# Kernel tuning notes

Hardware: AMD Instinct MI355X
Metric: run time of the kernel (lower is better)

The kernel has to match this reference:

```python
import jax, jax.numpy as jnp
import numpy as np

D_MODEL = 1024
N_HEADS = 16
D_K = D_MODEL // N_HEADS
D_FF = 4096
EPS = 1e-6
NEG = -1e9


def layer_norm(x, alpha, bias):
    # torch: mean/std over last dim, std is unbiased (ddof=1), eps added to std
    mean = jnp.mean(x, axis=-1, keepdims=True)
    std = jnp.std(x, axis=-1, keepdims=True, ddof=1)
    return alpha * (x - mean) / (std + EPS) + bias


def setup_inputs() -> dict:
    key = jax.random.key(0)
    ks = jax.random.split(key, 12)
    B, S = 2, 2048
    s_attn = 1.0 / np.sqrt(D_MODEL)
    s_ff1 = 1.0 / np.sqrt(D_MODEL)
    s_ff2 = 1.0 / np.sqrt(D_FF)
    inp = {
        "x": jax.random.normal(ks[0], (B, S, D_MODEL), jnp.float32),
        "mask": jnp.ones((1, 1, S, S), jnp.int32),
        "wq": jax.random.normal(ks[1], (D_MODEL, D_MODEL), jnp.float32) * s_attn,
        "bq": jnp.zeros((D_MODEL,), jnp.float32),
        "wk": jax.random.normal(ks[2], (D_MODEL, D_MODEL), jnp.float32) * s_attn,
        "bk": jnp.zeros((D_MODEL,), jnp.float32),
        "wv": jax.random.normal(ks[3], (D_MODEL, D_MODEL), jnp.float32) * s_attn,
        "bv": jnp.zeros((D_MODEL,), jnp.float32),
        "wo": jax.random.normal(ks[4], (D_MODEL, D_MODEL), jnp.float32) * s_attn,
        "bo": jnp.zeros((D_MODEL,), jnp.float32),
        "w1": jax.random.normal(ks[5], (D_MODEL, D_FF), jnp.float32) * s_ff1,
        "b1": jnp.zeros((D_FF,), jnp.float32),
        "w2": jax.random.normal(ks[6], (D_FF, D_MODEL), jnp.float32) * s_ff2,
        "b2": jnp.zeros((D_MODEL,), jnp.float32),
        "a1": jnp.ones((1,), jnp.float32),
        "c1": jnp.zeros((1,), jnp.float32),
        "a2": jnp.ones((1,), jnp.float32),
        "c2": jnp.zeros((1,), jnp.float32),
    }
    return inp


def reference(x, mask, wq, bq, wk, bk, wv, bv, wo, bo, w1, b1, w2, b2, a1, c1, a2, c2):
    B, S, D = x.shape

    def mha(h):
        q = (h @ wq + bq).reshape(B, S, N_HEADS, D_K).transpose(0, 2, 1, 3)
        k = (h @ wk + bk).reshape(B, S, N_HEADS, D_K).transpose(0, 2, 1, 3)
        v = (h @ wv + bv).reshape(B, S, N_HEADS, D_K).transpose(0, 2, 1, 3)
        scores = jnp.einsum('bhqd,bhkd->bhqk', q, k) / jnp.sqrt(jnp.float32(D_K))
        scores = jnp.where(mask == 0, jnp.float32(NEG), scores)
        weights = jax.nn.softmax(scores, axis=-1)
        out = jnp.einsum('bhqk,bhkd->bhqd', weights, v)
        out = out.transpose(0, 2, 1, 3).reshape(B, S, D)
        return out @ wo + bo

    def ffn(h):
        return jax.nn.relu(h @ w1 + b1) @ w2 + b2

    # pre-LN residual connections (dropout=0 / eval mode)
    x = x + mha(layer_norm(x, a1, c1))
    x = x + ffn(layer_norm(x, a2, c2))
    return x
```

## Files before the change

kernel.cpp:

```cpp
#include <hip/hip_runtime.h>
#include <hip/hip_bf16.h>
#include <type_traits>


typedef __attribute__((ext_vector_type(8))) short short8v;
typedef __attribute__((ext_vector_type(4))) float f32x4;
typedef __attribute__((ext_vector_type(4))) unsigned uint4v;

#define D_MODEL 1024
#define SEQ 2048
#define NROWS 4096

__device__ __forceinline__ short f2bs(float f) {
  __hip_bfloat16 h = __float2bfloat16(f);
  return __builtin_bit_cast(short, h);
}

__device__ __forceinline__ unsigned cvtpk(float lo, float hi) {
  unsigned r;
  asm("v_cvt_pk_bf16_f32 %0, %1, %2" : "=v"(r) : "v"(lo), "v"(hi));
  return r;
}

__device__ __forceinline__ void perm16swap(unsigned& a, unsigned& b) {
  asm volatile("v_permlane16_swap_b32 %0, %1" : "+v"(a), "+v"(b));
}

__device__ __forceinline__ void async_copy16(const void* g, void* l) {
  __builtin_amdgcn_global_load_lds(
      (__attribute__((address_space(1))) void*)g,
      (__attribute__((address_space(3))) void*)l,
      16, 0, 0);
}

__global__ __launch_bounds__(256)
void transpose4_bf16_kernel(const float* __restrict__ wq, const float* __restrict__ wk,
                            const float* __restrict__ wv, const float* __restrict__ wo,
                            short* __restrict__ oq, short* __restrict__ ow,
                            float qscale) {
  __shared__ float tile[32][33];
  const int z = blockIdx.z;
  const float* in = (z == 0) ? wq : (z == 1) ? wk : (z == 2) ? wv : wo;
  short* out = (z < 3) ? (oq + (size_t)z * 1024 * 1024) : ow;
  const float scale = (z == 0) ? qscale : 1.0f;
  const int n0 = blockIdx.x * 32, k0 = blockIdx.y * 32;
  const int tx = threadIdx.x, ty = threadIdx.y;
#pragma unroll
  for (int j = 0; j < 4; ++j)
    tile[ty + j * 8][tx] = in[(size_t)(k0 + ty + j * 8) * 1024 + n0 + tx];
  __syncthreads();
#pragma unroll
  for (int j = 0; j < 4; ++j)
    out[(size_t)(n0 + ty + j * 8) * 1024 + k0 + tx] = f2bs(tile[tx][ty + j * 8] * scale);
}

__global__ __launch_bounds__(256)
void transpose_ffn_kernel(const float* __restrict__ w1, const float* __restrict__ w2,
                          short* __restrict__ o1, short* __restrict__ o2) {
  __shared__ float tile[32][33];
  const int z = blockIdx.z;
  const float* in = z ? w2 : w1;
  short* out = z ? o2 : o1;
  const int K = z ? 4096 : 1024, N = z ? 1024 : 4096;
  const int n0 = (z ? blockIdx.y : blockIdx.x) * 32;
  const int k0 = (z ? blockIdx.x : blockIdx.y) * 32;
  const int tx = threadIdx.x, ty = threadIdx.y;
#pragma unroll
  for (int j = 0; j < 4; ++j)
    tile[ty + j * 8][tx] = in[(size_t)(k0 + ty + j * 8) * N + n0 + tx];
  __syncthreads();
#pragma unroll
  for (int j = 0; j < 4; ++j)
    out[(size_t)(n0 + ty + j * 8) * K + k0 + tx] = f2bs(tile[tx][ty + j * 8]);
}

__global__ __launch_bounds__(256)
void transpose_v_kernel(const short* __restrict__ qkv, short* __restrict__ vt) {
  __shared__ short tile[32][33];
  const int bh = blockIdx.z, b = bh >> 4, h = bh & 15;
  const int s0 = blockIdx.x * 32, d0 = blockIdx.y * 32;
  const int tx = threadIdx.x, ty = threadIdx.y;
  const short* src = qkv + ((size_t)b * SEQ) * 3072 + 2048 + h * 64;
#pragma unroll
  for (int j = 0; j < 4; ++j)
    tile[ty + j * 8][tx] = src[(size_t)(s0 + ty + j * 8) * 3072 + d0 + tx];
  __syncthreads();
  short* dst = vt + (size_t)bh * 64 * SEQ;
#pragma unroll
  for (int j = 0; j < 4; ++j)
    dst[(size_t)(d0 + ty + j * 8) * SEQ + s0 + tx] = tile[tx][ty + j * 8];
}

__global__ void concat_bias_kernel(const float* __restrict__ bq, const float* __restrict__ bk,
                                   const float* __restrict__ bv, float* __restrict__ outb,
                                   float qscale) {
  int i = blockIdx.x * 256 + threadIdx.x;
  float v = (i < 1024) ? bq[i] * qscale : (i < 2048 ? bk[i - 1024] : bv[i - 2048]);
  outb[i] = v;
}

__global__ __launch_bounds__(256)
void layernorm_kernel(const float* __restrict__ x, short* __restrict__ out,
                      const float* __restrict__ alpha, const float* __restrict__ beta) {
  const int row = blockIdx.x;
  const int t = threadIdx.x;
  float4 v = ((const float4*)(x + (size_t)row * D_MODEL))[t];
  float s = v.x + v.y + v.z + v.w;
  float sq = v.x * v.x + v.y * v.y + v.z * v.z + v.w * v.w;
#pragma unroll
  for (int m = 1; m < 64; m <<= 1) {
    s += __shfl_xor(s, m, 64);
    sq += __shfl_xor(sq, m, 64);
  }
  __shared__ float sh_s[4], sh_q[4];
  const int wid = t >> 6;
  if ((t & 63) == 0) { sh_s[wid] = s; sh_q[wid] = sq; }
  __syncthreads();
  s = sh_s[0] + sh_s[1] + sh_s[2] + sh_s[3];
  sq = sh_q[0] + sh_q[1] + sh_q[2] + sh_q[3];
  const float mean = s * (1.0f / 1024.0f);
  const float var = fmaxf(0.0f, (sq - 1024.0f * mean * mean) * (1.0f / 1023.0f));
  const float scl = alpha[0] / (sqrtf(var) + 1e-6f);
  const float sft = beta[0];
  short4 o;
  o.x = f2bs((v.x - mean) * scl + sft);
  o.y = f2bs((v.y - mean) * scl + sft);
  o.z = f2bs((v.z - mean) * scl + sft);
  o.w = f2bs((v.w - mean) * scl + sft);
  ((short4*)(out + (size_t)row * D_MODEL))[t] = o;
}

template <int MF, int NF, bool RELU, bool RESID, bool OUT_BF16>
__global__ __launch_bounds__(256)
void gemm_bt_sb_kernel(const short* __restrict__ A, const short* __restrict__ Bt,
                       const float* __restrict__ bias, const float* __restrict__ resid,
                       void* __restrict__ out, int M, int N, int K) {
  constexpr int BM = MF * 32, BN = NF * 32, BK = 64;
  __shared__ short As[BM * BK];
  __shared__ short Bs[BN * BK];
  const int tid = threadIdx.x;
  const int lane = tid & 63, wid = tid >> 6;
  const int wr = wid >> 1, wc = wid & 1;
  const int l15 = lane & 15, kg = lane >> 4;

  const int gx = gridDim.x;
  const int nwg = gx * gridDim.y;
  const int bid = blockIdx.y * gx + blockIdx.x;
  const int tilei = (bid & 7) * (nwg >> 3) + (bid >> 3);
  const int m0 = (tilei / gx) * BM, n0 = (tilei % gx) * BN;

  f32x4 acc[MF][NF];
#pragma unroll
  for (int m = 0; m < MF; ++m)
#pragma unroll
    for (int n = 0; n < NF; ++n) acc[m][n] = (f32x4){0.f, 0.f, 0.f, 0.f};

  const int r0 = tid >> 3, c0 = tid & 7;
  const int csw = (c0 ^ (r0 & 7)) << 3;
  const short* pa = A + (size_t)(m0 + r0) * K + csw;
  const short* pb = Bt + (size_t)(n0 + r0) * K + csw;

  const int NT = K / BK;
  for (int t = 0; t < NT; ++t) {
    const size_t ko = (size_t)t * BK;
#pragma unroll
    for (int it = 0; it < MF; ++it)
      async_copy16(pa + (size_t)it * 32 * K + ko, &As[(tid + it * 256) * 8]);
#pragma unroll
    for (int it = 0; it < NF; ++it)
      async_copy16(pb + (size_t)it * 32 * K + ko, &Bs[(tid + it * 256) * 8]);
    __syncthreads();

    short8v a[2][MF], b[2][NF];
#pragma unroll
    for (int m = 0; m < MF; ++m) {
      const int row = wr * MF * 16 + m * 16 + l15;
#pragma unroll
      for (int kt = 0; kt < 2; ++kt)
        a[kt][m] = *(const short8v*)&As[row * BK + (((kg + 4 * kt) ^ (row & 7)) << 3)];
    }
#pragma unroll
    for (int n = 0; n < NF; ++n) {
      const int row = wc * NF * 16 + n * 16 + l15;
#pragma unroll
      for (int kt = 0; kt < 2; ++kt)
        b[kt][n] = *(const short8v*)&Bs[row * BK + (((kg + 4 * kt) ^ (row & 7)) << 3)];
    }
    __builtin_amdgcn_s_setprio(1);
#pragma unroll
    for (int kt = 0; kt < 2; ++kt)
#pragma unroll
      for (int m = 0; m < MF; ++m)
#pragma unroll
        for (int n = 0; n < NF; ++n)
          acc[m][n] = __builtin_amdgcn_mfma_f32_16x16x32_bf16(a[kt][m], b[kt][n], acc[m][n], 0, 0, 0);
    __builtin_amdgcn_s_setprio(0);
    __syncthreads();
  }

#pragma unroll
  for (int m = 0; m < MF; ++m) {
#pragma unroll
    for (int n = 0; n < NF; ++n) {
      const int col = n0 + wc * NF * 16 + n * 16 + l15;
      const float bv = bias[col];
#pragma unroll
      for (int r = 0; r < 4; ++r) {
        const size_t row = (size_t)(m0 + wr * MF * 16 + m * 16 + kg * 4 + r);
        float v = acc[m][n][r] + bv;
        if (RELU) v = fmaxf(v, 0.0f);
        if (RESID) v += resid[row * N + col];
        if (OUT_BF16)
          ((short*)out)[row * N + col] = f2bs(v);
        else
          ((float*)out)[row * N + col] = v;
      }
    }
  }
}

template <bool RELU, bool RESID, bool OUT_BF16>
__global__ __launch_bounds__(256)
void gemm_bt_k64_kernel(const short* __restrict__ A, const short* __restrict__ Bt,
                        const float* __restrict__ bias, const float* __restrict__ resid,
                        void* __restrict__ out, int M, int N, int K) {
  constexpr int BM = 64, BN = 64, BK = 64;
  __shared__ short As[2][BM * BK];
  __shared__ short Bs[2][BN * BK];
  const int tid = threadIdx.x;
  const int lane = tid & 63, wid = tid >> 6;
  const int wr = wid >> 1, wc = wid & 1;
  const int l15 = lane & 15, kg = lane >> 4;

  const int gx = gridDim.x;
  const int nwg = gx * gridDim.y;
  const int bid = blockIdx.y * gx + blockIdx.x;
  const int tilei = (bid & 7) * (nwg >> 3) + (bid >> 3);
  const int m0 = (tilei / gx) * BM, n0 = (tilei % gx) * BN;

  f32x4 acc[2][2];
#pragma unroll
  for (int m = 0; m < 2; ++m)
#pragma unroll
    for (int n = 0; n < 2; ++n) acc[m][n] = (f32x4){0.f, 0.f, 0.f, 0.f};

  const int rA0 = tid >> 3, cA0 = (((tid & 7)) ^ (rA0 & 7)) << 3;
  const int rA1 = (tid + 256) >> 3, cA1 = (((tid + 256) & 7) ^ (rA1 & 7)) << 3;
  const short* pa0 = A + (size_t)(m0 + rA0) * K + cA0;
  const short* pa1 = A + (size_t)(m0 + rA1) * K + cA1;
  const short* pb0 = Bt + (size_t)(n0 + rA0) * K + cA0;
  const short* pb1 = Bt + (size_t)(n0 + rA1) * K + cA1;

  auto stage = [&](int buf, int t) {
    const size_t ko = (size_t)t * BK;
    async_copy16(pa0 + ko, &As[buf][tid * 8]);
    async_copy16(pa1 + ko, &As[buf][(tid + 256) * 8]);
    async_copy16(pb0 + ko, &Bs[buf][tid * 8]);
    async_copy16(pb1 + ko, &Bs[buf][(tid + 256) * 8]);
  };

  const int NT = K / BK;

  auto bodyk = [&](auto BUFC, int t) {
    constexpr int buf = decltype(BUFC)::value;
    if (t + 1 < NT) stage(buf ^ 1, t + 1);
    short8v a[2][2], b[2][2];
#pragma unroll
    for (int m = 0; m < 2; ++m) {
      const int row = wr * 32 + m * 16 + l15;
#pragma unroll
      for (int kt = 0; kt < 2; ++kt)
        a[kt][m] = *(const short8v*)&As[buf][row * BK + (((kg + 4 * kt) ^ (row & 7)) << 3)];
    }
#pragma unroll
    for (int n = 0; n < 2; ++n) {
      const int row = wc * 32 + n * 16 + l15;
#pragma unroll
      for (int kt = 0; kt < 2; ++kt)
        b[kt][n] = *(const short8v*)&Bs[buf][row * BK + (((kg + 4 * kt) ^ (row & 7)) << 3)];
    }
    __builtin_amdgcn_s_setprio(1);
#pragma unroll
    for (int kt = 0; kt < 2; ++kt)
#pragma unroll
      for (int m = 0; m < 2; ++m)
#pragma unroll
        for (int n = 0; n < 2; ++n)
          acc[m][n] = __builtin_amdgcn_mfma_f32_16x16x32_bf16(a[kt][m], b[kt][n], acc[m][n], 0, 0, 0);
    __builtin_amdgcn_s_setprio(0);
    __syncthreads();
  };

  stage(0, 0);
  __syncthreads();
  for (int t = 0; t < NT; t += 2) {
    bodyk(std::integral_constant<int, 0>{}, t);
    bodyk(std::integral_constant<int, 1>{}, t + 1);
  }

#pragma unroll
  for (int m = 0; m < 2; ++m) {
#pragma unroll
    for (int n = 0; n < 2; ++n) {
      const int col = n0 + wc * 32 + n * 16 + l15;
      const float bv = bias[col];
#pragma unroll
      for (int r = 0; r < 4; ++r) {
        const size_t row = (size_t)(m0 + wr * 32 + m * 16 + kg * 4 + r);
        float v = acc[m][n][r] + bv;
        if (RELU) v = fmaxf(v, 0.0f);
        if (RESID) v += resid[row * N + col];
        if (OUT_BF16)
          ((short*)out)[row * N + col] = f2bs(v);
        else
          ((float*)out)[row * N + col] = v;
      }
    }
  }
}

__global__ __launch_bounds__(256)
void attn_kernel(const short* __restrict__ qkv, const short* __restrict__ vt,
                 short* __restrict__ out) {
  const int bh = blockIdx.y;
  const int b = bh >> 4, h = bh & 15;
  const int q0 = blockIdx.x * 128;
  const int tid = threadIdx.x;
  const int lane = tid & 63, wid = tid >> 6;
  const int l15 = lane & 15, kg = lane >> 4;

  __shared__ short Ks[2][64 * 64];
  __shared__ short Vs[2][64 * 64];

  const size_t RS = 3072;
  const short* Qb = qkv + (size_t)b * SEQ * RS + h * 64;
  const short* Kb = Qb + 1024;
  const short* Vtb = vt + (size_t)bh * 64 * SEQ;

  short8v qf[2][2];
#pragma unroll
  for (int qi = 0; qi < 2; ++qi) {
    const short* qrow = Qb + (size_t)(q0 + wid * 32 + qi * 16 + l15) * RS + kg * 8;
    qf[qi][0] = *(const short8v*)(qrow);
    qf[qi][1] = *(const short8v*)(qrow + 32);
  }

  const int i0 = tid, i1 = tid + 256;
  const int r0 = i0 >> 3, b0 = (i0 & 7) ^ (r0 & 7);
  const int r1 = i1 >> 3, b1 = (i1 & 7) ^ (r1 & 7);
  const short* pk0 = Kb + (size_t)r0 * RS + b0 * 8;
  const short* pk1 = Kb + (size_t)r1 * RS + b1 * 8;
  const short* pv0 = Vtb + (size_t)r0 * SEQ + b0 * 8;
  const short* pv1 = Vtb + (size_t)r1 * SEQ + b1 * 8;

  auto stage = [&](int buf, int kv0) {
    async_copy16(pk0 + (size_t)kv0 * RS, &Ks[buf][i0 * 8]);
    async_copy16(pk1 + (size_t)kv0 * RS, &Ks[buf][i1 * 8]);
    async_copy16(pv0 + kv0, &Vs[buf][i0 * 8]);
    async_copy16(pv1 + kv0, &Vs[buf][i1 * 8]);
  };

  f32x4 o[2][4];
  f32x4 lacc[2];
#pragma unroll
  for (int qi = 0; qi < 2; ++qi) {
    lacc[qi] = (f32x4){0.f, 0.f, 0.f, 0.f};
#pragma unroll
    for (int i = 0; i < 4; ++i) o[qi][i] = (f32x4){0.f, 0.f, 0.f, 0.f};
  }

  const short ONE = 0x3F80;
  const short8v ones = {ONE, ONE, ONE, ONE, ONE, ONE, ONE, ONE};

  const int colblk = ((kg & 1) << 1) | (kg >> 1);

  auto tilebody = [&](auto BUFC, int kv_next, bool do_stage) {
    constexpr int buf = decltype(BUFC)::value;
    if (do_stage) stage(buf ^ 1, kv_next);

    f32x4 s[2][4];
    __builtin_amdgcn_s_setprio(1);
#pragma unroll
    for (int nt = 0; nt < 4; ++nt) {
      const int r = l15 + nt * 16, rx = r & 7;
      const short8v k0 = *(const short8v*)&Ks[buf][r * 64 + ((kg ^ rx) << 3)];
      const short8v k1 = *(const short8v*)&Ks[buf][r * 64 + (((kg + 4) ^ rx) << 3)];
#pragma unroll
      for (int qi = 0; qi < 2; ++qi) {
        f32x4 c = (f32x4){0.f, 0.f, 0.f, 0.f};
        c = __builtin_amdgcn_mfma_f32_16x16x32_bf16(k0, qf[qi][0], c, 0, 0, 0);
        c = __builtin_amdgcn_mfma_f32_16x16x32_bf16(k1, qf[qi][1], c, 0, 0, 0);
        s[qi][nt] = c;
      }
    }
    __builtin_amdgcn_s_setprio(0);

    unsigned w[2][4][2];
#pragma unroll
    for (int qi = 0; qi < 2; ++qi)
#pragma unroll
      for (int nt = 0; nt < 4; ++nt) {
        float p0 = __builtin_amdgcn_exp2f(s[qi][nt][0]);
        float p1 = __builtin_amdgcn_exp2f(s[qi][nt][1]);
        float p2 = __builtin_amdgcn_exp2f(s[qi][nt][2]);
        float p3 = __builtin_amdgcn_exp2f(s[qi][nt][3]);
        w[qi][nt][0] = cvtpk(p0, p1);
        w[qi][nt][1] = cvtpk(p2, p3);
      }

    __builtin_amdgcn_s_setprio(1);
#pragma unroll
    for (int kt = 0; kt < 2; ++kt) {
      short8v pf[2];
#pragma unroll
      for (int qi = 0; qi < 2; ++qi) {
        unsigned x0 = w[qi][2 * kt][0], y0 = w[qi][2 * kt + 1][0];
        unsigned x1 = w[qi][2 * kt][1], y1 = w[qi][2 * kt + 1][1];
        perm16swap(x0, y0);
        perm16swap(x1, y1);
        uint4v uv = {x0, x1, y0, y1};
        pf[qi] = __builtin_bit_cast(short8v, uv);
        lacc[qi] = __builtin_amdgcn_mfma_f32_16x16x32_bf16(ones, pf[qi], lacc[qi], 0, 0, 0);
      }
#pragma unroll
      for (int nt = 0; nt < 4; ++nt) {
        const int r = l15 + nt * 16;
        const short8v vf = *(const short8v*)&Vs[buf][r * 64 + (((colblk + 4 * kt) ^ (r & 7)) << 3)];
#pragma unroll
        for (int qi = 0; qi < 2; ++qi)
          o[qi][nt] = __builtin_amdgcn_mfma_f32_16x16x32_bf16(vf, pf[qi], o[qi][nt], 0, 0, 0);
      }
    }
    __builtin_amdgcn_s_setprio(0);

    __syncthreads();
  };

  stage(0, 0);
  __syncthreads();
  for (int kv0 = 0; kv0 < SEQ; kv0 += 128) {
    tilebody(std::integral_constant<int, 0>{}, kv0 + 64, true);
    tilebody(std::integral_constant<int, 1>{}, kv0 + 128, kv0 + 128 < SEQ);
  }

#pragma unroll
  for (int qi = 0; qi < 2; ++qi) {
    const float linv = 1.0f / lacc[qi][0];
    short* ob = out + ((size_t)b * SEQ + q0 + wid * 32 + qi * 16 + l15) * D_MODEL + h * 64;
#pragma unroll
    for (int nt = 0; nt < 4; ++nt) {
      short4 st;
      st.x = f2bs(o[qi][nt][0] * linv);
      st.y = f2bs(o[qi][nt][1] * linv);
      st.z = f2bs(o[qi][nt][2] * linv);
      st.w = f2bs(o[qi][nt][3] * linv);
      *(short4*)(ob + nt * 16 + kg * 4) = st;
    }
  }
}

static constexpr size_t OFF_WQKV = 0;
static constexpr size_t OFF_WO   = 6291456;
static constexpr size_t OFF_W1   = 8388608;
static constexpr size_t OFF_W2   = 16777216;
static constexpr size_t OFF_BQKV = 25165824;
static constexpr size_t OFF_H1   = 25178112;
static constexpr size_t OFF_QKV  = 33566720;
static constexpr size_t OFF_AO   = 58732544;
static constexpr size_t OFF_H2   = 67121152;
static constexpr size_t OFF_F1   = 75509760;
static constexpr size_t OFF_VT   = OFF_H1;

extern "C" void kernel_launch(void* const* d_in, const int* in_sizes, int n_in,
                              void* d_out, int out_size, void* d_ws, size_t ws_size,
                              hipStream_t stream) {
  const float* x  = (const float*)d_in[0];
  const float* wq = (const float*)d_in[2];
  const float* bq = (const float*)d_in[3];
  const float* wk = (const float*)d_in[4];
  const float* bk = (const float*)d_in[5];
  const float* wv = (const float*)d_in[6];
  const float* bv = (const float*)d_in[7];
  const float* wo = (const float*)d_in[8];
  const float* bo = (const float*)d_in[9];
  const float* w1 = (const float*)d_in[10];
  const float* b1 = (const float*)d_in[11];
  const float* w2 = (const float*)d_in[12];
  const float* b2 = (const float*)d_in[13];
  const float* a1 = (const float*)d_in[14];
  const float* c1 = (const float*)d_in[15];
  const float* a2 = (const float*)d_in[16];
  const float* c2 = (const float*)d_in[17];
  float* outp = (float*)d_out;
  char* ws = (char*)d_ws;

  short* wqkv_t = (short*)(ws + OFF_WQKV);
  short* wo_t   = (short*)(ws + OFF_WO);
  short* w1_t   = (short*)(ws + OFF_W1);
  short* w2_t   = (short*)(ws + OFF_W2);
  float* bqkv   = (float*)(ws + OFF_BQKV);
  short* h1     = (short*)(ws + OFF_H1);
  short* qkv    = (short*)(ws + OFF_QKV);
  short* ao     = (short*)(ws + OFF_AO);
  short* h2     = (short*)(ws + OFF_H2);
  short* f1     = (short*)(ws + OFF_F1);
  short* vtb    = (short*)(ws + OFF_VT);

  const float QSCALE = 0.125f * 1.44269504f;
  const dim3 tb(32, 8);
  transpose4_bf16_kernel<<<dim3(32, 32, 4), tb, 0, stream>>>(
      wq, wk, wv, wo, wqkv_t, wo_t, QSCALE);
  transpose_ffn_kernel<<<dim3(128, 32, 2), tb, 0, stream>>>(w1, w2, w1_t, w2_t);
  concat_bias_kernel<<<12, 256, 0, stream>>>(bq, bk, bv, bqkv, QSCALE);

  layernorm_kernel<<<NROWS, 256, 0, stream>>>(x, h1, a1, c1);
  gemm_bt_sb_kernel<4, 4, false, false, true><<<dim3(24, 32), 256, 0, stream>>>(
      h1, wqkv_t, bqkv, nullptr, qkv, NROWS, 3072, 1024);
  transpose_v_kernel<<<dim3(64, 2, 32), tb, 0, stream>>>(qkv, vtb);
  attn_kernel<<<dim3(16, 32), 256, 0, stream>>>(qkv, vtb, ao);
  gemm_bt_k64_kernel<false, true, false><<<dim3(16, 64), 256, 0, stream>>>(
      ao, wo_t, bo, x, d_out, NROWS, 1024, 1024);

  layernorm_kernel<<<NROWS, 256, 0, stream>>>(outp, h2, a2, c2);
  gemm_bt_sb_kernel<4, 4, true, false, true><<<dim3(32, 32), 256, 0, stream>>>(
      h2, w1_t, b1, nullptr, f1, NROWS, 4096, 1024);
  gemm_bt_k64_kernel<false, true, false><<<dim3(16, 64), 256, 0, stream>>>(
      f1, w2_t, b2, outp, d_out, NROWS, 1024, 4096);
}
```

Baseline: 225.1 us.

## Replace 64x64 output GEMM with intra-block K-split two-wave kernel

The N=1024 GEMMs (attention output projection and FFN down-projection) now use a 128-thread block in which each of two waves computes the full 64x64 tile over half of each 64-wide K slice. Each wave stages into its own LDS region, so the per-iteration __syncthreads is replaced by explicit vmcnt waits. The two partial accumulators are reduced through LDS at the end. This aims to remove block-wide barriers and raise MFMA work per LDS load. In exchange it halves the threads per block, raises accumulator register use, and adds an LDS reduction step.

Measured after the change: 278.2 us. +23.6%, slower.

```diff
diff --git a/kernel.cpp b/kernel.cpp
--- a/kernel.cpp
+++ b/kernel.cpp
@@ -220,93 +220,114 @@
 }
 
 template <bool RELU, bool RESID, bool OUT_BF16>
-__global__ __launch_bounds__(256)
-void gemm_bt_k64_kernel(const short* __restrict__ A, const short* __restrict__ Bt,
+__global__ __launch_bounds__(128)
+void gemm_ksplit_kernel(const short* __restrict__ A, const short* __restrict__ Bt,
                         const float* __restrict__ bias, const float* __restrict__ resid,
                         void* __restrict__ out, int M, int N, int K) {
-  constexpr int BM = 64, BN = 64, BK = 64;
-  __shared__ short As[2][BM * BK];
-  __shared__ short Bs[2][BN * BK];
+  __shared__ short As[2][2][2048];
+  __shared__ short Bs[2][2][2048];
   const int tid = threadIdx.x;
-  const int lane = tid & 63, wid = tid >> 6;
-  const int wr = wid >> 1, wc = wid & 1;
+  const int lane = tid & 63, w = tid >> 6;
   const int l15 = lane & 15, kg = lane >> 4;
+  const int s = (l15 >> 1) & 3;
 
   const int gx = gridDim.x;
   const int nwg = gx * gridDim.y;
   const int bid = blockIdx.y * gx + blockIdx.x;
   const int tilei = (bid & 7) * (nwg >> 3) + (bid >> 3);
-  const int m0 = (tilei / gx) * BM, n0 = (tilei % gx) * BN;
-
-  f32x4 acc[2][2];
-#pragma unroll
-  for (int m = 0; m < 2; ++m)
-#pragma unroll
-    for (int n = 0; n < 2; ++n) acc[m][n] = (f32x4){0.f, 0.f, 0.f, 0.f};
-
-  const int rA0 = tid >> 3, cA0 = (((tid & 7)) ^ (rA0 & 7)) << 3;
-  const int rA1 = (tid + 256) >> 3, cA1 = (((tid + 256) & 7) ^ (rA1 & 7)) << 3;
-  const short* pa0 = A + (size_t)(m0 + rA0) * K + cA0;
-  const short* pa1 = A + (size_t)(m0 + rA1) * K + cA1;
-  const short* pb0 = Bt + (size_t)(n0 + rA0) * K + cA0;
-  const short* pb1 = Bt + (size_t)(n0 + rA1) * K + cA1;
+  const int m0 = (tilei / gx) * 64, n0 = (tilei % gx) * 64;
+
+  f32x4 acc[4][4];
+#pragma unroll
+  for (int m = 0; m < 4; ++m)
+#pragma unroll
+    for (int n = 0; n < 4; ++n) acc[m][n] = (f32x4){0.f, 0.f, 0.f, 0.f};
+
+  const int rr = lane >> 2, cc = lane & 3;
+  const short* pA[4];
+  const short* pB[4];
+#pragma unroll
+  for (int i = 0; i < 4; ++i) {
+    const int r = i * 16 + rr;
+    const int csw = ((cc ^ ((r >> 1) & 3)) << 3) + w * 32;
+    pA[i] = A + (size_t)(m0 + r) * K + csw;
+    pB[i] = Bt + (size_t)(n0 + r) * K + csw;
+  }
+  short* lA = &As[w][0][0];
+  short* lB = &Bs[w][0][0];
+
+  const int NT = K / 64;
 
   auto stage = [&](int buf, int t) {
-    const size_t ko = (size_t)t * BK;
-    async_copy16(pa0 + ko, &As[buf][tid * 8]);
-    async_copy16(pa1 + ko, &As[buf][(tid + 256) * 8]);
-    async_copy16(pb0 + ko, &Bs[buf][tid * 8]);
-    async_copy16(pb1 + ko, &Bs[buf][(tid + 256) * 8]);
+    const size_t ko = (size_t)t * 64;
+#pragma unroll
+    for (int i = 0; i < 4; ++i)
+      async_copy16(pA[i] + ko, lA + buf * 2048 + (i * 64 + lane) * 8);
+#pragma unroll
+    for (int i = 0; i < 4; ++i)
+      async_copy16(pB[i] + ko, lB + buf * 2048 + (i * 64 + lane) * 8);
   };
-
-  const int NT = K / BK;
 
   auto bodyk = [&](auto BUFC, int t) {
     constexpr int buf = decltype(BUFC)::value;
-    if (t + 1 < NT) stage(buf ^ 1, t + 1);
-    short8v a[2][2], b[2][2];
-#pragma unroll
-    for (int m = 0; m < 2; ++m) {
-      const int row = wr * 32 + m * 16 + l15;
-#pragma unroll
-      for (int kt = 0; kt < 2; ++kt)
-        a[kt][m] = *(const short8v*)&As[buf][row * BK + (((kg + 4 * kt) ^ (row & 7)) << 3)];
-    }
-#pragma unroll
-    for (int n = 0; n < 2; ++n) {
-      const int row = wc * 32 + n * 16 + l15;
-#pragma unroll
-      for (int kt = 0; kt < 2; ++kt)
-        b[kt][n] = *(const short8v*)&Bs[buf][row * BK + (((kg + 4 * kt) ^ (row & 7)) << 3)];
+    if (t + 1 < NT) {
+      stage(buf ^ 1, t + 1);
+      asm volatile("s_waitcnt vmcnt(8)" ::: "memory");
+    } else {
+      asm volatile("s_waitcnt vmcnt(0)" ::: "memory");
+    }
+    __builtin_amdgcn_sched_barrier(0);
+    short8v a[4], b[4];
+#pragma unroll
+    for (int m = 0; m < 4; ++m) {
+      const int row = m * 16 + l15;
+      a[m] = *(const short8v*)&lA[buf * 2048 + row * 32 + ((kg ^ s) << 3)];
+      b[m] = *(const short8v*)&lB[buf * 2048 + row * 32 + ((kg ^ s) << 3)];
     }
     __builtin_amdgcn_s_setprio(1);
 #pragma unroll
-    for (int kt = 0; kt < 2; ++kt)
-#pragma unroll
-      for (int m = 0; m < 2; ++m)
-#pragma unroll
-        for (int n = 0; n < 2; ++n)
-          acc[m][n] = __builtin_amdgcn_mfma_f32_16x16x32_bf16(a[kt][m], b[kt][n], acc[m][n], 0, 0, 0);
+    for (int m = 0; m < 4; ++m)
+#pragma unroll
+      for (int n = 0; n < 4; ++n)
+        acc[m][n] = __builtin_amdgcn_mfma_f32_16x16x32_bf16(a[m], b[n], acc[m][n], 0, 0, 0);
     __builtin_amdgcn_s_setprio(0);
-    __syncthreads();
   };
 
   stage(0, 0);
-  __syncthreads();
   for (int t = 0; t < NT; t += 2) {
     bodyk(std::integral_constant<int, 0>{}, t);
     bodyk(std::integral_constant<int, 1>{}, t + 1);
   }
 
-#pragma unroll
-  for (int m = 0; m < 2; ++m) {
-#pragma unroll
-    for (int n = 0; n < 2; ++n) {
-      const int col = n0 + wc * 32 + n * 16 + l15;
+  float* ex = (float*)&As[0][0][0];
+  __syncthreads();
+#pragma unroll
+  for (int mo = 0; mo < 2; ++mo)
+#pragma unroll
+    for (int n = 0; n < 4; ++n) {
+      const int slot = (mo * 4 + n) * 256 + kg * 64 + l15 * 4;
+      *(f32x4*)&ex[w * 2048 + slot] = acc[2 * (1 - w) + mo][n];
+    }
+  __syncthreads();
+#pragma unroll
+  for (int mo = 0; mo < 2; ++mo)
+#pragma unroll
+    for (int n = 0; n < 4; ++n) {
+      const int slot = (mo * 4 + n) * 256 + kg * 64 + l15 * 4;
+      f32x4 p = *(const f32x4*)&ex[(1 - w) * 2048 + slot];
+      acc[2 * w + mo][n] += p;
+    }
+
+#pragma unroll
+  for (int mo = 0; mo < 2; ++mo) {
+    const int m = 2 * w + mo;
+#pragma unroll
+    for (int n = 0; n < 4; ++n) {
+      const int col = n0 + n * 16 + l15;
       const float bv = bias[col];
 #pragma unroll
       for (int r = 0; r < 4; ++r) {
-        const size_t row = (size_t)(m0 + wr * 32 + m * 16 + kg * 4 + r);
+        const size_t row = (size_t)(m0 + m * 16 + kg * 4 + r);
         float v = acc[m][n][r] + bv;
         if (RELU) v = fmaxf(v, 0.0f);
         if (RESID) v += resid[row * N + col];
@@ -518,12 +539,12 @@
       h1, wqkv_t, bqkv, nullptr, qkv, NROWS, 3072, 1024);
   transpose_v_kernel<<<dim3(64, 2, 32), tb, 0, stream>>>(qkv, vtb);
   attn_kernel<<<dim3(16, 32), 256, 0, stream>>>(qkv, vtb, ao);
-  gemm_bt_k64_kernel<false, true, false><<<dim3(16, 64), 256, 0, stream>>>(
+  gemm_ksplit_kernel<false, true, false><<<dim3(16, 64), 128, 0, stream>>>(
       ao, wo_t, bo, x, d_out, NROWS, 1024, 1024);
 
   layernorm_kernel<<<NROWS, 256, 0, stream>>>(outp, h2, a2, c2);
   gemm_bt_sb_kernel<4, 4, true, false, true><<<dim3(32, 32), 256, 0, stream>>>(
       h2, w1_t, b1, nullptr, f1, NROWS, 4096, 1024);
-  gemm_bt_k64_kernel<false, true, false><<<dim3(16, 64), 256, 0, stream>>>(
+  gemm_ksplit_kernel<false, true, false><<<dim3(16, 64), 128, 0, stream>>>(
       f1, w2_t, b2, outp, d_out, NROWS, 1024, 4096);
 }
```
